# Performance work log

Hardware: AMD Instinct MI355X
Metric: run time of the kernel (lower is better)

The kernel has to match this reference:

```python
import jax, jax.numpy as jnp
import numpy as np

H, V, B, T = 2048, 32000, 8, 256
G = 4          # num_generations per reward group
BETA = 0.1     # KL coefficient
EPS = 1e-4


def setup_inputs() -> dict:
    key = jax.random.key(0)
    ks = jax.random.split(key, 6)
    scale = 1.0 / np.sqrt(H)  # keep logits O(1) so exp() in KL is finite
    return {
        "x": jax.random.normal(ks[0], (B, T, H), jnp.float32),
        "weight": jax.random.normal(ks[1], (V, H), jnp.float32) * scale,
        "attention_mask": jax.random.randint(ks[2], (B, T), 0, 2).astype(jnp.int32),
        "rewards": jax.random.normal(ks[3], (B,), jnp.float32),
        "ref_input": jax.random.normal(ks[4], (B, T, H), jnp.float32),
        "ref_weight": jax.random.normal(ks[5], (V, H), jnp.float32) * scale,
    }


def _gather_token_logps(inp, w, tokens):
    # log-softmax over vocab, then gather at `tokens`  -> (B, T)
    logits = jnp.einsum('bth,vh->btv', inp, w)
    logp = jax.nn.log_softmax(logits, axis=-1)
    return jnp.take_along_axis(logp, tokens[..., None], axis=-1)[..., 0]


def reference(x, weight, attention_mask, rewards, ref_input, ref_weight):
    # policy logits / log-probs  (B, T, V)
    logits = jnp.einsum('bth,vh->btv', x, weight)
    logp = jax.nn.log_softmax(logits, axis=-1)
    # chosen tokens = argmax of policy logits (as in the Liger test harness)
    tokens = jnp.argmax(logits, axis=-1)                                   # (B, T) int
    tok_logp = jnp.take_along_axis(logp, tokens[..., None], axis=-1)[..., 0]  # (B, T)

    # reference model log-probs at the same tokens (no grad)
    ref_tok_logp = jax.lax.stop_gradient(
        _gather_token_logps(ref_input, ref_weight, tokens))               # (B, T)

    # group-relative advantages (groups of G generations, unbiased std as torch.std)
    r = rewards.reshape(-1, G)
    mean_g = jnp.repeat(r.mean(axis=1), G)                                # (B,)
    std_g = jnp.repeat(r.std(axis=1, ddof=1), G)                          # (B,)
    adv = (rewards - mean_g) / (std_g + EPS)                              # (B,)

    # ratio = exp(logp - logp.detach()) == 1 in value, carries grad of logp
    per_tok = jnp.exp(tok_logp - jax.lax.stop_gradient(tok_logp)) * adv[:, None]
    # k3 KL estimator vs reference policy
    kl = jnp.exp(ref_tok_logp - tok_logp) - (ref_tok_logp - tok_logp) - 1.0
    per_tok = per_tok - BETA * kl

    mask = attention_mask.astype(jnp.float32)
    loss = -(per_tok * mask).sum() / mask.sum()
    mean_kl = ((kl * mask).sum(axis=1) / mask.sum(axis=1)).mean()
    return loss, mean_kl
```

## Files before the change

### kernel.cpp

```cpp
#include <hip/hip_runtime.h>
#include <hip/hip_bf16.h>
#include <math.h>

#define H_DIM 2048
#define V_DIM 32000
#define BT    2048
#define TM    128
#define TN    128
#define TK    32
#define NKT   (H_DIM / TK)
#define NBLK  (V_DIM / TN)
#define BETA  0.1f
#define EPSR  1e-4f

typedef __attribute__((ext_vector_type(8))) short bf16x8;
typedef __attribute__((ext_vector_type(4))) float f32x4;


__device__ __forceinline__ unsigned pack_bf16x2(float a, float b) {
    unsigned ua = __float_as_uint(a) + 0x8000u;
    unsigned ub = __float_as_uint(b) + 0x8000u;
    return __builtin_amdgcn_perm(ub, ua, 0x07060302u);
}

__device__ __forceinline__ void merge_ms(float& m, float& s, float m2, float s2) {
    float nm = fmaxf(m, m2);
    s = s * __expf(m - nm) + s2 * __expf(m2 - nm);
    m = nm;
}

__device__ __forceinline__ void gl_lds16(const void* g, void* l) {
    __builtin_amdgcn_global_load_lds(
        (const __attribute__((address_space(1))) void*)g,
        (__attribute__((address_space(3))) void*)l, 16, 0, 0);
}

__global__ __launch_bounds__(256) void pack_kernel(
    const float* __restrict__ src, uint4* __restrict__ dst)
{
    __shared__ float tile[128 * 40];
    const int t  = threadIdx.x;
    const int rt = blockIdx.x, kt = blockIdx.y;

    #pragma unroll
    for (int it = 0; it < 4; it++) {
        int idx = (it * 256 + t) * 4;
        int row = idx >> 5, k = idx & 31;
        float4 v = *(const float4*)(src + (size_t)(rt * 128 + row) * H_DIM + kt * 32 + k);
        *(float4*)(tile + row * 40 + k) = v;
    }
    __syncthreads();

    uint4* d = dst + ((size_t)(rt * 64 + kt) << 9);
    #pragma unroll
    for (int it = 0; it < 2; it++) {
        int c = it * 256 + t;
        int kq = c >> 7, row = c & 127;
        const float* p = tile + row * 40 + kq * 8;
        d[c] = make_uint4(pack_bf16x2(p[0], p[1]), pack_bf16x2(p[2], p[3]),
                          pack_bf16x2(p[4], p[5]), pack_bf16x2(p[6], p[7]));
    }
}

__global__ __launch_bounds__(256) void gemm_lse_fast(
    const ushort* __restrict__ Ap, const ushort* __restrict__ Wp,
    const ushort* __restrict__ Rp, const ushort* __restrict__ RWp,
    float4* __restrict__ part, float4* __restrict__ part2)
{
    __shared__ char smem[16384];
    float* redM = (float*)smem;
    float* redS = (float*)(smem + 1024);
    int*   redC = (int*)  (smem + 2048);

    const int tid  = threadIdx.x;
    const int lane = tid & 63;
    const int wv   = tid >> 6;
    const int wm   = wv >> 1, wn = wv & 1;
    const int q    = lane >> 4, cl = lane & 15;

    const int mb = blockIdx.x, nb = blockIdx.y;
    const ushort* A  = blockIdx.z ? Rp  : Ap;
    const ushort* Bw = blockIdx.z ? RWp : Wp;
    float4* pp = blockIdx.z ? part2 : part;

    const ushort* gs = (wv < 2 ? A + (size_t)mb * 64 * 4096
                               : Bw + (size_t)nb * 64 * 4096)
                       + (size_t)(wv & 1) * 4 * 512 + lane * 8;
    char* ls = smem + (wv < 2 ? 0 : 8192) + (wv & 1) * 4 * 1024 + lane * 16;

    f32x4 acc[4][4];
    const f32x4 zero = {0.f, 0.f, 0.f, 0.f};
    #pragma unroll
    for (int i = 0; i < 4; i++)
        #pragma unroll
        for (int j = 0; j < 4; j++) acc[i][j] = zero;

    for (int kt = 0; kt < NKT; kt++) {
        #pragma unroll
        for (int c = 0; c < 4; c++) gl_lds16(gs + c * 512, ls + c * 1024);
        gs += 4096;
        __syncthreads();

        bf16x8 af[4], bfr[4];
        #pragma unroll
        for (int i = 0; i < 4; i++) {
            af[i]  = *(const bf16x8*)(smem + (q * 128 + wm * 64 + i * 16 + cl) * 16);
            bfr[i] = *(const bf16x8*)(smem + 8192 + (q * 128 + wn * 64 + i * 16 + cl) * 16);
        }
        #pragma unroll
        for (int i = 0; i < 4; i++)
            #pragma unroll
            for (int j = 0; j < 4; j++)
                acc[i][j] = __builtin_amdgcn_mfma_f32_16x16x32_bf16(af[i], bfr[j], acc[i][j], 0, 0, 0);
        __syncthreads();
    }

    #pragma unroll
    for (int ti = 0; ti < 4; ti++) {
        #pragma unroll
        for (int r = 0; r < 4; r++) {
            float vals[4];
            #pragma unroll
            for (int j = 0; j < 4; j++) vals[j] = acc[ti][j][r];
            float m = vals[0]; int cj = 0;
            #pragma unroll
            for (int j = 1; j < 4; j++) if (vals[j] > m) { m = vals[j]; cj = j; }
            float s = 0.f;
            #pragma unroll
            for (int j = 0; j < 4; j++) s += __expf(vals[j] - m);
            int cidx = wn * 64 + cj * 16 + cl;
            #pragma unroll
            for (int off = 1; off < 16; off <<= 1) {
                float m2 = __shfl_xor(m, off);
                float s2 = __shfl_xor(s, off);
                int   c2 = __shfl_xor(cidx, off);
                float nm = fmaxf(m, m2);
                s = s * __expf(m - nm) + s2 * __expf(m2 - nm);
                if (m2 > m || (m2 == m && c2 < cidx)) cidx = c2;
                m = nm;
            }
            int rloc = wm * 64 + ti * 16 + q * 4 + r;
            if (cl == 0) { redM[rloc*2+wn] = m; redS[rloc*2+wn] = s; redC[rloc*2+wn] = cidx; }
        }
    }
    __syncthreads();
    if (tid < TM) {
        float ma = redM[tid*2+0], mb2 = redM[tid*2+1];
        float sa = redS[tid*2+0], sb  = redS[tid*2+1];
        int   ca = redC[tid*2+0], cb  = redC[tid*2+1];
        float nm = fmaxf(ma, mb2);
        float s  = sa * __expf(ma - nm) + sb * __expf(mb2 - nm);
        int   cc = (mb2 > ma || (mb2 == ma && cb < ca)) ? cb : ca;
        pp[(size_t)(mb * TM + tid) * NBLK + nb] =
            make_float4(nm, s, __int_as_float(nb * TN + cc), 0.f);
    }
}

__global__ __launch_bounds__(256) void gemm_lse_fallback(
    const float* __restrict__ A, const float* __restrict__ Bw,
    float4* __restrict__ part, const int* __restrict__ token,
    float* __restrict__ gather_out)
{
    __shared__ char smem[TM*TK*2 + TN*TK*2];
    ushort* sA = (ushort*)smem;
    ushort* sB = (ushort*)(smem + TM*TK*2);
    float* redM   = (float*)smem;
    float* redS   = (float*)(smem + 1024);
    int*   redC   = (int*)  (smem + 2048);
    int*   tokloc = (int*)  (smem + 3072);

    const int tid  = threadIdx.x;
    const int lane = tid & 63;
    const int wv   = tid >> 6;
    const int wm   = wv >> 1, wn = wv & 1;
    const int q    = lane >> 4, cl = lane & 15;
    const int m0 = blockIdx.x * TM;
    const int n0 = blockIdx.y * TN;
    const int nb = blockIdx.y;

    const int srow = tid >> 1, sseg = tid & 1;
    const float4* gA = (const float4*)(A  + (size_t)(m0 + srow) * H_DIM) + sseg * 4;
    const float4* gB = (const float4*)(Bw + (size_t)(n0 + srow) * H_DIM) + sseg * 4;
    uint4* wA = (uint4*)sA + srow * 4 + sseg * 2;
    uint4* wB = (uint4*)sB + srow * 4 + sseg * 2;

    f32x4 acc[4][4];
    const f32x4 zero = {0.f, 0.f, 0.f, 0.f};
    #pragma unroll
    for (int i = 0; i < 4; i++)
        #pragma unroll
        for (int j = 0; j < 4; j++) acc[i][j] = zero;

    float4 ra0 = gA[0], ra1 = gA[1], ra2 = gA[2], ra3 = gA[3];
    float4 rb0 = gB[0], rb1 = gB[1], rb2 = gB[2], rb3 = gB[3];

    for (int kt = 0; kt < H_DIM; kt += TK) {
        wA[0] = make_uint4(pack_bf16x2(ra0.x,ra0.y), pack_bf16x2(ra0.z,ra0.w),
                           pack_bf16x2(ra1.x,ra1.y), pack_bf16x2(ra1.z,ra1.w));
        wA[1] = make_uint4(pack_bf16x2(ra2.x,ra2.y), pack_bf16x2(ra2.z,ra2.w),
                           pack_bf16x2(ra3.x,ra3.y), pack_bf16x2(ra3.z,ra3.w));
        wB[0] = make_uint4(pack_bf16x2(rb0.x,rb0.y), pack_bf16x2(rb0.z,rb0.w),
                           pack_bf16x2(rb1.x,rb1.y), pack_bf16x2(rb1.z,rb1.w));
        wB[1] = make_uint4(pack_bf16x2(rb2.x,rb2.y), pack_bf16x2(rb2.z,rb2.w),
                           pack_bf16x2(rb3.x,rb3.y), pack_bf16x2(rb3.z,rb3.w));
        __syncthreads();
        if (kt + TK < H_DIM) {
            int kq = (kt + TK) >> 2;
            ra0 = gA[kq]; ra1 = gA[kq+1]; ra2 = gA[kq+2]; ra3 = gA[kq+3];
            rb0 = gB[kq]; rb1 = gB[kq+1]; rb2 = gB[kq+2]; rb3 = gB[kq+3];
        }
        bf16x8 af[4], bfr[4];
        #pragma unroll
        for (int i = 0; i < 4; i++) {
            af[i]  = *(const bf16x8*)(sA + (wm*64 + i*16 + cl) * TK + q*8);
            bfr[i] = *(const bf16x8*)(sB + (wn*64 + i*16 + cl) * TK + q*8);
        }
        #pragma unroll
        for (int i = 0; i < 4; i++)
            #pragma unroll
            for (int j = 0; j < 4; j++)
                acc[i][j] = __builtin_amdgcn_mfma_f32_16x16x32_bf16(af[i], bfr[j], acc[i][j], 0, 0, 0);
        __syncthreads();
    }

    #pragma unroll
    for (int ti = 0; ti < 4; ti++) {
        #pragma unroll
        for (int r = 0; r < 4; r++) {
            float vals[4];
            #pragma unroll
            for (int j = 0; j < 4; j++) vals[j] = acc[ti][j][r];
            float m = vals[0]; int cj = 0;
            #pragma unroll
            for (int j = 1; j < 4; j++) if (vals[j] > m) { m = vals[j]; cj = j; }
            float s = 0.f;
            #pragma unroll
            for (int j = 0; j < 4; j++) s += __expf(vals[j] - m);
            int cidx = wn*64 + cj*16 + cl;
            #pragma unroll
            for (int off = 1; off < 16; off <<= 1) {
                float m2 = __shfl_xor(m, off);
                float s2 = __shfl_xor(s, off);
                int   c2 = __shfl_xor(cidx, off);
                float nm = fmaxf(m, m2);
                s = s * __expf(m - nm) + s2 * __expf(m2 - nm);
                if (m2 > m || (m2 == m && c2 < cidx)) cidx = c2;
                m = nm;
            }
            int rloc = wm*64 + ti*16 + q*4 + r;
            if (cl == 0) { redM[rloc*2+wn] = m; redS[rloc*2+wn] = s; redC[rloc*2+wn] = cidx; }
        }
    }
    __syncthreads();
    if (tid < TM) {
        float ma = redM[tid*2+0], mb = redM[tid*2+1];
        float sa = redS[tid*2+0], sb = redS[tid*2+1];
        int   ca = redC[tid*2+0], cb = redC[tid*2+1];
        float nm = fmaxf(ma, mb);
        float s  = sa * __expf(ma - nm) + sb * __expf(mb - nm);
        int   cc = (mb > ma || (mb == ma && cb < ca)) ? cb : ca;
        part[(size_t)(m0 + tid) * NBLK + nb] = make_float4(nm, s, __int_as_float(n0 + cc), 0.f);
    }

    if (token != nullptr) {
        if (tid < TM) tokloc[tid] = token[m0 + tid] - n0;
        __syncthreads();
        #pragma unroll
        for (int ti = 0; ti < 4; ti++) {
            #pragma unroll
            for (int r = 0; r < 4; r++) {
                int rloc = wm*64 + ti*16 + q*4 + r;
                int tl = tokloc[rloc];
                if (tl >= 0 && tl < TN && ((tl >> 6) & 1) == wn && (tl & 15) == cl) {
                    int tjm = (tl >> 4) & 3;
                    float v = acc[ti][0][r];
                    if (tjm == 1) v = acc[ti][1][r];
                    if (tjm == 2) v = acc[ti][2][r];
                    if (tjm == 3) v = acc[ti][3][r];
                    gather_out[m0 + rloc] = v;
                }
            }
        }
    }
}


__global__ __launch_bounds__(256) void reduce_policy_kernel(
    const float4* __restrict__ part, int* __restrict__ token, float* __restrict__ tok_logp)
{
    int row = blockIdx.x, t = threadIdx.x;
    float m = -3.0e38f, s = 0.f; int cc = 0x7fffffff;
    if (t < NBLK) { float4 p = part[(size_t)row * NBLK + t]; m = p.x; s = p.y; cc = __float_as_int(p.z); }
    for (int off = 1; off < 64; off <<= 1) {
        float m2 = __shfl_xor(m, off);
        float s2 = __shfl_xor(s, off);
        int   c2 = __shfl_xor(cc, off);
        float nm = fmaxf(m, m2);
        s = s * __expf(m - nm) + s2 * __expf(m2 - nm);
        if (m2 > m || (m2 == m && c2 < cc)) cc = c2;
        m = nm;
    }
    __shared__ float smM[4], smS[4]; __shared__ int smC[4];
    if ((t & 63) == 0) { smM[t>>6] = m; smS[t>>6] = s; smC[t>>6] = cc; }
    __syncthreads();
    if (t == 0) {
        m = smM[0]; s = smS[0]; cc = smC[0];
        for (int i = 1; i < 4; i++) {
            float m2 = smM[i], s2 = smS[i]; int c2 = smC[i];
            float nm = fmaxf(m, m2);
            s = s * __expf(m - nm) + s2 * __expf(m2 - nm);
            if (m2 > m || (m2 == m && c2 < cc)) cc = c2;
            m = nm;
        }
        token[row] = cc;
        tok_logp[row] = -__logf(s);
    }
}

__global__ __launch_bounds__(256) void dot_gather_kernel(
    const float* __restrict__ rx, const float* __restrict__ rw,
    const int* __restrict__ token, float* __restrict__ out)
{
    int row = blockIdx.x, t = threadIdx.x;
    const float4* a = (const float4*)(rx + (size_t)row * H_DIM);
    const float4* b = (const float4*)(rw + (size_t)token[row] * H_DIM);
    float4 a0 = a[t*2], a1 = a[t*2+1], b0 = b[t*2], b1 = b[t*2+1];
    float s = a0.x*b0.x + a0.y*b0.y + a0.z*b0.z + a0.w*b0.w
            + a1.x*b1.x + a1.y*b1.y + a1.z*b1.z + a1.w*b1.w;
    for (int off = 1; off < 64; off <<= 1) s += __shfl_xor(s, off);
    __shared__ float ss[4];
    if ((t & 63) == 0) ss[t >> 6] = s;
    __syncthreads();
    if (t == 0) out[row] = ss[0] + ss[1] + ss[2] + ss[3];
}

__global__ __launch_bounds__(256) void reduce_ref_kernel(
    const float4* __restrict__ part, const float* __restrict__ tok_logp,
    const float* __restrict__ gathered, float* __restrict__ klrow)
{
    int row = blockIdx.x, t = threadIdx.x;
    float m = -3.0e38f, s = 0.f;
    if (t < NBLK) { float4 p = part[(size_t)row * NBLK + t]; m = p.x; s = p.y; }
    for (int off = 1; off < 64; off <<= 1) {
        float m2 = __shfl_xor(m, off), s2 = __shfl_xor(s, off);
        merge_ms(m, s, m2, s2);
    }
    __shared__ float smM[4], smS[4];
    if ((t & 63) == 0) { smM[t>>6] = m; smS[t>>6] = s; }
    __syncthreads();
    if (t == 0) {
        m = smM[0]; s = smS[0];
        for (int i = 1; i < 4; i++) merge_ms(m, s, smM[i], smS[i]);
        float lse = m + __logf(s);
        float d = (gathered[row] - lse) - tok_logp[row];
        klrow[row] = __expf(d) - d - 1.0f;
    }
}

__global__ __launch_bounds__(256) void final_kernel(
    const int* __restrict__ amask, const float* __restrict__ rewards,
    const float* __restrict__ klrow, float* __restrict__ out)
{
    int t = threadIdx.x;
    int b = t >> 5;
    int g = b >> 2;
    float r0 = rewards[g*4+0], r1 = rewards[g*4+1], r2 = rewards[g*4+2], r3 = rewards[g*4+3];
    float mean = 0.25f * (r0 + r1 + r2 + r3);
    float var = ((r0-mean)*(r0-mean) + (r1-mean)*(r1-mean) +
                 (r2-mean)*(r2-mean) + (r3-mean)*(r3-mean)) * (1.0f/3.0f);
    float adv = (rewards[b] - mean) / (sqrtf(var) + EPSR);

    float ln = 0.f, ms = 0.f, kb = 0.f, mb = 0.f;
    for (int i = 0; i < 8; i++) {
        int row = t*8 + i;
        float mk = (float)amask[row];
        float kl = klrow[row];
        ln += (adv - BETA * kl) * mk;
        ms += mk;
        kb += kl * mk;
        mb += mk;
    }
    __shared__ float sLN[256], sMS[256], sKB[256], sMB[256], sKLb[8];
    sLN[t] = ln; sMS[t] = ms; sKB[t] = kb; sMB[t] = mb;
    __syncthreads();
    if (t < 8) {
        float skb = 0.f, smb = 0.f;
        for (int i = 0; i < 32; i++) { skb += sKB[t*32+i]; smb += sMB[t*32+i]; }
        sKLb[t] = skb / smb;
    }
    __syncthreads();
    if (t == 0) {
        float lnt = 0.f, mst = 0.f;
        for (int i = 0; i < 256; i++) { lnt += sLN[i]; mst += sMS[i]; }
        float mkl = 0.f;
        for (int i = 0; i < 8; i++) mkl += sKLb[i];
        out[0] = -lnt / mst;
        out[1] = mkl * 0.125f;
    }
}


extern "C" void kernel_launch(void* const* d_in, const int* in_sizes, int n_in,
                              void* d_out, int out_size, void* d_ws, size_t ws_size,
                              hipStream_t stream)
{
    const float* x       = (const float*)d_in[0];
    const float* w       = (const float*)d_in[1];
    const int*   amask   = (const int*)  d_in[2];
    const float* rewards = (const float*)d_in[3];
    const float* rx      = (const float*)d_in[4];
    const float* rw      = (const float*)d_in[5];
    float* out = (float*)d_out;
    char* ws = (char*)d_ws;

    const size_t W_P  = (size_t)V_DIM * H_DIM * 2;
    const size_t A_P  = (size_t)BT * H_DIM * 2;
    const size_t PART = (size_t)BT * NBLK * 16;
    const size_t NEED = 2*W_P + 2*A_P + 2*PART + 4*8192;

    if (ws_size >= NEED) {
        ushort* Wp   = (ushort*)(ws);
        ushort* RWp  = (ushort*)(ws + W_P);
        ushort* Ap   = (ushort*)(ws + 2*W_P);
        ushort* Rp   = (ushort*)(ws + 2*W_P + A_P);
        float4* part  = (float4*)(ws + 2*W_P + 2*A_P);
        float4* part2 = (float4*)(ws + 2*W_P + 2*A_P + PART);
        char*   tail  =          ws + 2*W_P + 2*A_P + 2*PART;
        int*   token    = (int*)  (tail);
        float* tok_logp = (float*)(tail + 8192);
        float* gathered = (float*)(tail + 16384);
        float* klrow    = (float*)(tail + 24576);

        pack_kernel<<<dim3(BT/128,  NKT), 256, 0, stream>>>(x,  (uint4*)Ap);
        pack_kernel<<<dim3(V_DIM/128, NKT), 256, 0, stream>>>(w,  (uint4*)Wp);
        pack_kernel<<<dim3(BT/128,  NKT), 256, 0, stream>>>(rx, (uint4*)Rp);
        pack_kernel<<<dim3(V_DIM/128, NKT), 256, 0, stream>>>(rw, (uint4*)RWp);

        gemm_lse_fast<<<dim3(BT/TM, NBLK, 2), 256, 0, stream>>>(Ap, Wp, Rp, RWp, part, part2);

        reduce_policy_kernel<<<BT, 256, 0, stream>>>(part, token, tok_logp);
        dot_gather_kernel<<<BT, 256, 0, stream>>>(rx, rw, token, gathered);
        reduce_ref_kernel<<<BT, 256, 0, stream>>>(part2, tok_logp, gathered, klrow);
        final_kernel<<<1, 256, 0, stream>>>(amask, rewards, klrow, out);
    } else {
        float4* part     = (float4*)ws;
        int*    token    = (int*)  (ws + PART);
        float*  tok_logp = (float*)(ws + PART + 8192);
        float*  gathered = (float*)(ws + PART + 16384);
        float*  klrow    = (float*)(ws + PART + 24576);

        dim3 g(BT / TM, NBLK), blk(256);
        gemm_lse_fallback<<<g, blk, 0, stream>>>(x, w, part, nullptr, nullptr);
        reduce_policy_kernel<<<BT, 256, 0, stream>>>(part, token, tok_logp);
        gemm_lse_fallback<<<g, blk, 0, stream>>>(rx, rw, part, token, gathered);
        reduce_ref_kernel<<<BT, 256, 0, stream>>>(part, tok_logp, gathered, klrow);
        final_kernel<<<1, 256, 0, stream>>>(amask, rewards, klrow, out);
    }
}
```

Baseline: 1.363 ms.

## Double GEMM K-step per barrier, drop LDS from pack, fuse tail reductions

The bf16 GEMM main loop now loads two 32-wide K slices (32 KB of LDS) per barrier pair, which halves the number of syncthreads and lets more loads be in flight. The pack kernel now converts straight from global memory to the packed layout without an LDS transpose. The policy reduction, reference dot gather and reference reduction are merged into one tail kernel, so there are fewer launches and intermediates. The larger LDS footprint may reduce occupancy of the GEMM.

```diff
diff --git a/kernel.cpp b/kernel.cpp
--- a/kernel.cpp
+++ b/kernel.cpp
@@ -7,8 +7,7 @@
 #define BT    2048
 #define TM    128
 #define TN    128
-#define TK    32
-#define NKT   (H_DIM / TK)
+#define NKT   (H_DIM / 32)
 #define NBLK  (V_DIM / TN)
 #define BETA  0.1f
 #define EPSR  1e-4f
@@ -38,27 +37,20 @@
 __global__ __launch_bounds__(256) void pack_kernel(
     const float* __restrict__ src, uint4* __restrict__ dst)
 {
-    __shared__ float tile[128 * 40];
     const int t  = threadIdx.x;
     const int rt = blockIdx.x, kt = blockIdx.y;
+    const int kq = t & 3;
+    const int r0 = t >> 2;
+    uint4* d = dst + ((size_t)(rt * 64 + kt) << 9);
 
     #pragma unroll
-    for (int it = 0; it < 4; it++) {
-        int idx = (it * 256 + t) * 4;
-        int row = idx >> 5, k = idx & 31;
-        float4 v = *(const float4*)(src + (size_t)(rt * 128 + row) * H_DIM + kt * 32 + k);
-        *(float4*)(tile + row * 40 + k) = v;
-    }
-    __syncthreads();
-
-    uint4* d = dst + ((size_t)(rt * 64 + kt) << 9);
-    #pragma unroll
-    for (int it = 0; it < 2; it++) {
-        int c = it * 256 + t;
-        int kq = c >> 7, row = c & 127;
-        const float* p = tile + row * 40 + kq * 8;
-        d[c] = make_uint4(pack_bf16x2(p[0], p[1]), pack_bf16x2(p[2], p[3]),
-                          pack_bf16x2(p[4], p[5]), pack_bf16x2(p[6], p[7]));
+    for (int half = 0; half < 2; half++) {
+        int row = r0 + half * 64;
+        const float* p = src + (size_t)(rt * 128 + row) * H_DIM + kt * 32 + kq * 8;
+        float4 v0 = *(const float4*)(p);
+        float4 v1 = *(const float4*)(p + 4);
+        d[kq * 128 + row] = make_uint4(pack_bf16x2(v0.x, v0.y), pack_bf16x2(v0.z, v0.w),
+                                       pack_bf16x2(v1.x, v1.y), pack_bf16x2(v1.z, v1.w));
     }
 }
 
@@ -67,7 +59,7 @@
     const ushort* __restrict__ Rp, const ushort* __restrict__ RWp,
     float4* __restrict__ part, float4* __restrict__ part2)
 {
-    __shared__ char smem[16384];
+    __shared__ char smem[32768];
     float* redM = (float*)smem;
     float* redS = (float*)(smem + 1024);
     int*   redC = (int*)  (smem + 2048);
@@ -85,8 +77,8 @@
 
     const ushort* gs = (wv < 2 ? A + (size_t)mb * 64 * 4096
                                : Bw + (size_t)nb * 64 * 4096)
-                       + (size_t)(wv & 1) * 4 * 512 + lane * 8;
-    char* ls = smem + (wv < 2 ? 0 : 8192) + (wv & 1) * 4 * 1024 + lane * 16;
+                       + (size_t)(wv & 1) * 4096 + lane * 8;
+    char* ls = smem + (wv < 2 ? 0 : 16384) + (wv & 1) * 8192 + lane * 16;
 
     f32x4 acc[4][4];
     const f32x4 zero = {0.f, 0.f, 0.f, 0.f};
@@ -95,23 +87,28 @@
         #pragma unroll
         for (int j = 0; j < 4; j++) acc[i][j] = zero;
 
-    for (int kt = 0; kt < NKT; kt++) {
-        #pragma unroll
-        for (int c = 0; c < 4; c++) gl_lds16(gs + c * 512, ls + c * 1024);
-        gs += 4096;
+    for (int kt = 0; kt < NKT / 2; kt++) {
+        #pragma unroll
+        for (int c = 0; c < 8; c++) gl_lds16(gs + c * 512, ls + c * 1024);
+        gs += 8192;
         __syncthreads();
 
-        bf16x8 af[4], bfr[4];
-        #pragma unroll
-        for (int i = 0; i < 4; i++) {
-            af[i]  = *(const bf16x8*)(smem + (q * 128 + wm * 64 + i * 16 + cl) * 16);
-            bfr[i] = *(const bf16x8*)(smem + 8192 + (q * 128 + wn * 64 + i * 16 + cl) * 16);
-        }
-        #pragma unroll
-        for (int i = 0; i < 4; i++)
-            #pragma unroll
-            for (int j = 0; j < 4; j++)
-                acc[i][j] = __builtin_amdgcn_mfma_f32_16x16x32_bf16(af[i], bfr[j], acc[i][j], 0, 0, 0);
+        #pragma unroll
+        for (int kk = 0; kk < 2; kk++) {
+            bf16x8 af[4], bfr[4];
+            #pragma unroll
+            for (int i = 0; i < 4; i++) {
+                af[i]  = *(const bf16x8*)(smem + kk * 8192
+                            + (q * 128 + wm * 64 + i * 16 + cl) * 16);
+                bfr[i] = *(const bf16x8*)(smem + 16384 + kk * 8192
+                            + (q * 128 + wn * 64 + i * 16 + cl) * 16);
+            }
+            #pragma unroll
+            for (int i = 0; i < 4; i++)
+                #pragma unroll
+                for (int j = 0; j < 4; j++)
+                    acc[i][j] = __builtin_amdgcn_mfma_f32_16x16x32_bf16(af[i], bfr[j], acc[i][j], 0, 0, 0);
+        }
         __syncthreads();
     }
 
@@ -156,14 +153,82 @@
     }
 }
 
+__global__ __launch_bounds__(256) void tail_kernel(
+    const float4* __restrict__ part, const float4* __restrict__ part2,
+    const float* __restrict__ rx, const float* __restrict__ rw,
+    float* __restrict__ klrow)
+{
+    int row = blockIdx.x, t = threadIdx.x;
+    __shared__ float smM[4], smS[4], sred[4];
+    __shared__ int smC[4];
+    __shared__ int s_token;
+    __shared__ float s_tok_logp;
+
+    float m = -3.0e38f, s = 0.f; int cc = 0x7fffffff;
+    if (t < NBLK) { float4 p = part[(size_t)row * NBLK + t]; m = p.x; s = p.y; cc = __float_as_int(p.z); }
+    for (int off = 1; off < 64; off <<= 1) {
+        float m2 = __shfl_xor(m, off);
+        float s2 = __shfl_xor(s, off);
+        int   c2 = __shfl_xor(cc, off);
+        float nm = fmaxf(m, m2);
+        s = s * __expf(m - nm) + s2 * __expf(m2 - nm);
+        if (m2 > m || (m2 == m && c2 < cc)) cc = c2;
+        m = nm;
+    }
+    if ((t & 63) == 0) { smM[t>>6] = m; smS[t>>6] = s; smC[t>>6] = cc; }
+    __syncthreads();
+    if (t == 0) {
+        m = smM[0]; s = smS[0]; cc = smC[0];
+        for (int i = 1; i < 4; i++) {
+            float m2 = smM[i], s2 = smS[i]; int c2 = smC[i];
+            float nm = fmaxf(m, m2);
+            s = s * __expf(m - nm) + s2 * __expf(m2 - nm);
+            if (m2 > m || (m2 == m && c2 < cc)) cc = c2;
+            m = nm;
+        }
+        s_token = cc;
+        s_tok_logp = -__logf(s);
+    }
+    __syncthreads();
+    int token = s_token;
+
+    {
+        const float4* a = (const float4*)(rx + (size_t)row * H_DIM);
+        const float4* b = (const float4*)(rw + (size_t)token * H_DIM);
+        float4 a0 = a[t*2], a1 = a[t*2+1], b0 = b[t*2], b1 = b[t*2+1];
+        float sd = a0.x*b0.x + a0.y*b0.y + a0.z*b0.z + a0.w*b0.w
+                 + a1.x*b1.x + a1.y*b1.y + a1.z*b1.z + a1.w*b1.w;
+        for (int off = 1; off < 64; off <<= 1) sd += __shfl_xor(sd, off);
+        if ((t & 63) == 0) sred[t >> 6] = sd;
+    }
+
+    float m3 = -3.0e38f, s3 = 0.f;
+    if (t < NBLK) { float4 p = part2[(size_t)row * NBLK + t]; m3 = p.x; s3 = p.y; }
+    for (int off = 1; off < 64; off <<= 1) {
+        float m2 = __shfl_xor(m3, off), s2 = __shfl_xor(s3, off);
+        merge_ms(m3, s3, m2, s2);
+    }
+    __syncthreads();
+    if ((t & 63) == 0) { smM[t>>6] = m3; smS[t>>6] = s3; }
+    __syncthreads();
+    if (t == 0) {
+        m3 = smM[0]; s3 = smS[0];
+        for (int i = 1; i < 4; i++) merge_ms(m3, s3, smM[i], smS[i]);
+        float lse = m3 + __logf(s3);
+        float gathered = sred[0] + sred[1] + sred[2] + sred[3];
+        float d = (gathered - lse) - s_tok_logp;
+        klrow[row] = __expf(d) - d - 1.0f;
+    }
+}
+
 __global__ __launch_bounds__(256) void gemm_lse_fallback(
     const float* __restrict__ A, const float* __restrict__ Bw,
     float4* __restrict__ part, const int* __restrict__ token,
     float* __restrict__ gather_out)
 {
-    __shared__ char smem[TM*TK*2 + TN*TK*2];
+    __shared__ char smem[16384];
     ushort* sA = (ushort*)smem;
-    ushort* sB = (ushort*)(smem + TM*TK*2);
+    ushort* sB = (ushort*)(smem + 8192);
     float* redM   = (float*)smem;
     float* redS   = (float*)(smem + 1024);
     int*   redC   = (int*)  (smem + 2048);
@@ -194,7 +259,7 @@
     float4 ra0 = gA[0], ra1 = gA[1], ra2 = gA[2], ra3 = gA[3];
     float4 rb0 = gB[0], rb1 = gB[1], rb2 = gB[2], rb3 = gB[3];
 
-    for (int kt = 0; kt < H_DIM; kt += TK) {
+    for (int kt = 0; kt < H_DIM; kt += 32) {
         wA[0] = make_uint4(pack_bf16x2(ra0.x,ra0.y), pack_bf16x2(ra0.z,ra0.w),
                            pack_bf16x2(ra1.x,ra1.y), pack_bf16x2(ra1.z,ra1.w));
         wA[1] = make_uint4(pack_bf16x2(ra2.x,ra2.y), pack_bf16x2(ra2.z,ra2.w),
@@ -204,16 +269,16 @@
         wB[1] = make_uint4(pack_bf16x2(rb2.x,rb2.y), pack_bf16x2(rb2.z,rb2.w),
                            pack_bf16x2(rb3.x,rb3.y), pack_bf16x2(rb3.z,rb3.w));
         __syncthreads();
-        if (kt + TK < H_DIM) {
-            int kq = (kt + TK) >> 2;
+        if (kt + 32 < H_DIM) {
+            int kq = (kt + 32) >> 2;
             ra0 = gA[kq]; ra1 = gA[kq+1]; ra2 = gA[kq+2]; ra3 = gA[kq+3];
             rb0 = gB[kq]; rb1 = gB[kq+1]; rb2 = gB[kq+2]; rb3 = gB[kq+3];
         }
         bf16x8 af[4], bfr[4];
         #pragma unroll
         for (int i = 0; i < 4; i++) {
-            af[i]  = *(const bf16x8*)(sA + (wm*64 + i*16 + cl) * TK + q*8);
-            bfr[i] = *(const bf16x8*)(sB + (wn*64 + i*16 + cl) * TK + q*8);
+            af[i]  = *(const bf16x8*)(sA + (wm*64 + i*16 + cl) * 32 + q*8);
+            bfr[i] = *(const bf16x8*)(sB + (wn*64 + i*16 + cl) * 32 + q*8);
         }
         #pragma unroll
         for (int i = 0; i < 4; i++)
@@ -317,23 +382,6 @@
     }
 }
 
-__global__ __launch_bounds__(256) void dot_gather_kernel(
-    const float* __restrict__ rx, const float* __restrict__ rw,
-    const int* __restrict__ token, float* __restrict__ out)
-{
-    int row = blockIdx.x, t = threadIdx.x;
-    const float4* a = (const float4*)(rx + (size_t)row * H_DIM);
-    const float4* b = (const float4*)(rw + (size_t)token[row] * H_DIM);
-    float4 a0 = a[t*2], a1 = a[t*2+1], b0 = b[t*2], b1 = b[t*2+1];
-    float s = a0.x*b0.x + a0.y*b0.y + a0.z*b0.z + a0.w*b0.w
-            + a1.x*b1.x + a1.y*b1.y + a1.z*b1.z + a1.w*b1.w;
-    for (int off = 1; off < 64; off <<= 1) s += __shfl_xor(s, off);
-    __shared__ float ss[4];
-    if ((t & 63) == 0) ss[t >> 6] = s;
-    __syncthreads();
-    if (t == 0) out[row] = ss[0] + ss[1] + ss[2] + ss[3];
-}
-
 __global__ __launch_bounds__(256) void reduce_ref_kernel(
     const float4* __restrict__ part, const float* __restrict__ tok_logp,
     const float* __restrict__ gathered, float* __restrict__ klrow)
@@ -426,21 +474,16 @@
         float4* part  = (float4*)(ws + 2*W_P + 2*A_P);
         float4* part2 = (float4*)(ws + 2*W_P + 2*A_P + PART);
         char*   tail  =          ws + 2*W_P + 2*A_P + 2*PART;
-        int*   token    = (int*)  (tail);
-        float* tok_logp = (float*)(tail + 8192);
-        float* gathered = (float*)(tail + 16384);
-        float* klrow    = (float*)(tail + 24576);
-
-        pack_kernel<<<dim3(BT/128,  NKT), 256, 0, stream>>>(x,  (uint4*)Ap);
+        float* klrow  = (float*)(tail);
+
+        pack_kernel<<<dim3(BT/128,    NKT), 256, 0, stream>>>(x,  (uint4*)Ap);
         pack_kernel<<<dim3(V_DIM/128, NKT), 256, 0, stream>>>(w,  (uint4*)Wp);
-        pack_kernel<<<dim3(BT/128,  NKT), 256, 0, stream>>>(rx, (uint4*)Rp);
+        pack_kernel<<<dim3(BT/128,    NKT), 256, 0, stream>>>(rx, (uint4*)Rp);
         pack_kernel<<<dim3(V_DIM/128, NKT), 256, 0, stream>>>(rw, (uint4*)RWp);
 
         gemm_lse_fast<<<dim3(BT/TM, NBLK, 2), 256, 0, stream>>>(Ap, Wp, Rp, RWp, part, part2);
 
-        reduce_policy_kernel<<<BT, 256, 0, stream>>>(part, token, tok_logp);
-        dot_gather_kernel<<<BT, 256, 0, stream>>>(rx, rw, token, gathered);
-        reduce_ref_kernel<<<BT, 256, 0, stream>>>(part2, tok_logp, gathered, klrow);
+        tail_kernel<<<BT, 256, 0, stream>>>(part, part2, rx, rw, klrow);
         final_kernel<<<1, 256, 0, stream>>>(amask, rewards, klrow, out);
     } else {
         float4* part     = (float4*)ws;
```

After: 1.408 ms. +3.3%, slower.
